# Optimization experiments

Measured on AMD Instinct MI355X. Metric: run time of the kernel, lower is better.

## Reference

```python
import jax, jax.numpy as jnp
import numpy as np

# Predictive-coding graph message passing (PCGraphConv core compute).
# Single-graph edge list (edge_src -> edge_dst) with one scalar weight per edge,
# tiled over the batch (weights.repeat(1, batchsize) in the original).
# PredictionMessagePassing: mu_i = sum_{e: dst(e)=i} w_e * f(x_{src(e)})
# ValueMessagePassing:      dx_j = -eps_j + f'(x_j) * sum_{e: src(e)=j} w_e * eps_{dst(e)}
# with eps = x - mu and f = tanh.

N_PER_GRAPH = 4096
E_PER_GRAPH = 524288
BATCH = 32


def setup_inputs() -> dict:
    key = jax.random.key(0)
    k1, k2, k3, k4 = jax.random.split(key, 4)
    x = jax.random.normal(k1, (BATCH * N_PER_GRAPH,), dtype=jnp.float32)
    weights = jax.random.normal(k2, (E_PER_GRAPH,), dtype=jnp.float32) * (1.0 / np.sqrt(N_PER_GRAPH))
    edge_src = jax.random.randint(k3, (E_PER_GRAPH,), 0, N_PER_GRAPH, dtype=jnp.int32)
    edge_dst = jax.random.randint(k4, (E_PER_GRAPH,), 0, N_PER_GRAPH, dtype=jnp.int32)
    return {"x": x, "weights": weights, "edge_src": edge_src, "edge_dst": edge_dst,
            "batch_size": BATCH, "num_vertices": N_PER_GRAPH}


def reference(x, weights, edge_src, edge_dst, batch_size, num_vertices):
    B, N = batch_size, num_vertices
    BN = B * N
    # Tile single-graph edges across the batch with per-graph node offsets.
    offs = (jnp.arange(B, dtype=edge_src.dtype) * N)[:, None]        # [B,1]
    src = (edge_src[None, :] + offs).reshape(-1)                     # [B*E]
    dst = (edge_dst[None, :] + offs).reshape(-1)                     # [B*E]
    w = jnp.tile(weights, B)                                         # [B*E]

    fx = jnp.tanh(x)                                                 # f(x)
    # Predictions: gather f(x) at src, weight per edge, scatter-add at dst.
    mu = jax.ops.segment_sum(w * fx[src], dst, num_segments=BN)      # [B*N]
    eps = x - mu                                                     # errors
    fprime = 1.0 - fx * fx                                           # f'(x)
    # Value update: backward flow of errors along edges.
    dx = -eps + fprime * jax.ops.segment_sum(w * eps[dst], src, num_segments=BN)
    return jnp.stack([mu, dx])                                       # [2, B*N]
```

## Files before the change

### kernel.cpp

```cpp
#include <hip/hip_runtime.h>


static constexpr int kB = 32, kLogB = 5;
static constexpr int kBkt = 256;
static constexpr int kNPB = 16;
static constexpr int kChunk = 2048;
static constexpr int kTile = 2560;

__global__ void __launch_bounds__(1024) k_hist(
    const int* __restrict__ esrc, const int* __restrict__ edst,
    const float* __restrict__ x, float* __restrict__ x_t,
    float* __restrict__ fx_t, unsigned* __restrict__ cntA,
    unsigned* __restrict__ cntB, int N, int E, int nBB) {
  __shared__ unsigned hA[kBkt], hB[kBkt];
  __shared__ float tile[32][65];
  int tid = threadIdx.x, blk = blockIdx.x;
  if (blk < nBB) {
    if (tid < kBkt) { hA[tid] = 0u; hB[tid] = 0u; }
    __syncthreads();
    int e0 = blk * kChunk, len = min(kChunk, E - e0);
    for (int i = tid; i < len; i += 1024) {
      atomicAdd(&hA[((unsigned)edst[e0 + i]) >> 4], 1u);
      atomicAdd(&hB[((unsigned)esrc[e0 + i]) >> 4], 1u);
    }
    __syncthreads();
    if (tid < kBkt) {
      cntA[(size_t)blk * kBkt + tid] = hA[tid];
      cntB[(size_t)blk * kBkt + tid] = hB[tid];
    }
  } else if (blk - nBB < (N >> 6)) {
    int n0 = (blk - nBB) * 64;
    for (int k = tid; k < 32 * 64; k += 1024) {
      int b = k >> 6, n = k & 63;
      tile[b][n] = x[b * N + n0 + n];
    }
    __syncthreads();
    for (int k = tid; k < 64 * 32; k += 1024) {
      int n = k >> 5, b = k & 31;
      float xv = tile[b][n];
      int j = (n0 + n) * kB + b;
      x_t[j] = xv;
      fx_t[j] = tanhf(xv);
    }
  }
}

__global__ void __launch_bounds__(1024) k_scan(
    const unsigned* __restrict__ cntA, const unsigned* __restrict__ cntB,
    unsigned* __restrict__ baseA, unsigned* __restrict__ baseB,
    unsigned* __restrict__ segA, unsigned* __restrict__ segB, int nBB) {
  __shared__ unsigned qoff[4][kBkt];
  __shared__ unsigned tot[kBkt];
  __shared__ unsigned bb[kBkt];
  const unsigned* cnt = blockIdx.x ? cntB : cntA;
  unsigned* base = blockIdx.x ? baseB : baseA;
  unsigned* seg  = blockIdx.x ? segB  : segA;
  int tid = threadIdx.x;
  int t = tid & (kBkt - 1), q = tid >> 8;
  int qlen = (nBB + 3) >> 2;
  int b0 = q * qlen;
  unsigned run = 0;
  for (int j = 0; j < qlen; j += 8) {
    unsigned c[8];
#pragma unroll
    for (int u = 0; u < 8; ++u) {
      int bi = b0 + j + u;
      c[u] = (bi < nBB) ? cnt[(size_t)bi * kBkt + t] : 0u;
    }
#pragma unroll
    for (int u = 0; u < 8; ++u) run += c[u];
  }
  qoff[q][t] = run;
  __syncthreads();
  unsigned myTot = 0;
  if (tid < kBkt) {
    unsigned p0 = qoff[0][tid], p1 = qoff[1][tid];
    unsigned p2 = qoff[2][tid], p3 = qoff[3][tid];
    qoff[0][tid] = 0u; qoff[1][tid] = p0;
    qoff[2][tid] = p0 + p1; qoff[3][tid] = p0 + p1 + p2;
    myTot = p0 + p1 + p2 + p3;
    tot[tid] = myTot;
  }
  __syncthreads();
  for (int o = 1; o < kBkt; o <<= 1) {
    unsigned v = 0;
    if (tid < kBkt && tid >= o) v = tot[tid - o];
    __syncthreads();
    if (tid < kBkt && tid >= o) tot[tid] += v;
    __syncthreads();
  }
  if (tid < kBkt) {
    unsigned excl = tot[tid] - myTot;
    bb[tid] = excl;
    seg[tid] = excl;
    if (tid == kBkt - 1) seg[kBkt] = excl + myTot;
  }
  __syncthreads();
  run = bb[t] + qoff[q][t];
  for (int j = 0; j < qlen; j += 8) {
    unsigned c[8];
#pragma unroll
    for (int u = 0; u < 8; ++u) {
      int bi = b0 + j + u;
      c[u] = (bi < nBB) ? cnt[(size_t)bi * kBkt + t] : 0u;
    }
#pragma unroll
    for (int u = 0; u < 8; ++u) {
      int bi = b0 + j + u;
      if (bi < nBB) base[(size_t)bi * kBkt + t] = run;
      run += c[u];
    }
  }
}

__global__ void __launch_bounds__(1024) k_scatter(
    const int* __restrict__ esrc, const int* __restrict__ edst,
    const float* __restrict__ wgt,
    const unsigned* __restrict__ cntA, const unsigned* __restrict__ cntB,
    const unsigned* __restrict__ baseA, const unsigned* __restrict__ baseB,
    uint2* __restrict__ recA, uint2* __restrict__ recB, int E, int nBB) {
  __shared__ unsigned myBase[kBkt], cntL[kBkt], baseL[kBkt], cnt2[kBkt];
  __shared__ uint2 cmp[kChunk];
  __shared__ unsigned char bktid[kChunk];
  int tid = threadIdx.x, blk = blockIdx.x;
  int e0 = blk * kChunk, len = min(kChunk, E - e0);
  for (int dir = 0; dir < 2; ++dir) {
    const int* key = dir ? esrc : edst;
    const int* oth = dir ? edst : esrc;
    const unsigned* cnt = dir ? cntB : cntA;
    const unsigned* base = dir ? baseB : baseA;
    uint2* out = dir ? recB : recA;
    if (tid < kBkt) {
      myBase[tid] = base[(size_t)blk * kBkt + tid];
      cntL[tid] = cnt[(size_t)blk * kBkt + tid];
      cnt2[tid] = 0u;
    }
    __syncthreads();
    if (tid < 64) {
      int qq = tid << 2;
      unsigned c0 = cntL[qq], c1 = cntL[qq + 1];
      unsigned c2 = cntL[qq + 2], c3 = cntL[qq + 3];
      unsigned s = c0 + c1 + c2 + c3, run = s;
#pragma unroll
      for (int o = 1; o < 64; o <<= 1) {
        unsigned v = __shfl_up(run, o, 64);
        if (tid >= o) run += v;
      }
      unsigned bse = run - s;
      baseL[qq] = bse; baseL[qq + 1] = bse + c0;
      baseL[qq + 2] = bse + c0 + c1; baseL[qq + 3] = bse + c0 + c1 + c2;
    }
    __syncthreads();
    for (int i = tid; i < len; i += 1024) {
      unsigned ky = (unsigned)key[e0 + i], ot = (unsigned)oth[e0 + i];
      unsigned bbk = ky >> 4;
      unsigned slot = baseL[bbk] + atomicAdd(&cnt2[bbk], 1u);
      cmp[slot] = make_uint2((ot << 4) | (ky & 15u), __float_as_uint(wgt[e0 + i]));
      bktid[slot] = (unsigned char)bbk;
    }
    __syncthreads();
    for (int s = tid; s < len; s += 1024) {
      unsigned bbk = bktid[s];
      out[myBase[bbk] + ((unsigned)s - baseL[bbk])] = cmp[s];
    }
    __syncthreads();
  }
}

__global__ void __launch_bounds__(1024) k_pass(
    const uint2* __restrict__ rec, const unsigned* __restrict__ seg,
    const float* __restrict__ vals, const float* __restrict__ x_t,
    const float* __restrict__ fx_t, float* __restrict__ eps_t,
    float* __restrict__ out, int N, int mode) {
  __shared__ uint2 srt[kTile];
  __shared__ unsigned hW[16 * kNPB];
  __shared__ unsigned wbase[16 * kNPB];
  __shared__ unsigned wcur[16 * kNPB];
  __shared__ unsigned h[kNPB], hb[kNPB];
  __shared__ float red[1024];
  int tid = threadIdx.x, t = blockIdx.x;
  int segb = (int)seg[t], sege = (int)seg[t + 1];
  int wv = tid >> 6;
  int b = tid & 31, hw = tid >> 5, l = hw >> 1, part = hw & 1;
  float acc = 0.0f;

  for (int t0 = segb; t0 < sege; t0 += kTile) {
    int len = min(kTile, sege - t0);
    if (tid < 16 * kNPB) { hW[tid] = 0u; wcur[tid] = 0u; }
    __syncthreads();
    for (int i = tid; i < len; i += 1024)
      atomicAdd(&hW[wv * kNPB + (rec[t0 + i].x & 15u)], 1u);
    __syncthreads();
    if (tid < kNPB) {
      unsigned run = 0;
#pragma unroll
      for (int w2 = 0; w2 < 16; ++w2) {
        unsigned c = hW[w2 * kNPB + tid];
        wbase[w2 * kNPB + tid] = run;
        run += c;
      }
      h[tid] = run;
    }
    __syncthreads();
    if (tid == 0) {
      unsigned run = 0;
#pragma unroll
      for (int l2 = 0; l2 < kNPB; ++l2) { hb[l2] = run; run += h[l2]; }
    }
    __syncthreads();
    if (tid < 16 * kNPB) wbase[tid] += hb[tid & (kNPB - 1)];
    __syncthreads();
    for (int i = tid; i < len; i += 1024) {
      uint2 r = rec[t0 + i];
      unsigned lx = r.x & 15u;
      srt[wbase[wv * kNPB + lx] + atomicAdd(&wcur[wv * kNPB + lx], 1u)] = r;
    }
    __syncthreads();

    int beg = (int)hb[l] + part, end = (int)hb[l] + (int)h[l];
    int last = end - 1; if (last < 0) last = 0;
    uint2 r0, r1, r2, r3, r4, r5, r6, r7;
    float v0, v1, v2, v3, v4, v5, v6, v7;
#define PC_LOAD(d)                                                   \
    { int p = beg + 2 * (d); uint2 rr = srt[min(p, last)];           \
      r##d = rr; v##d = vals[(((rr.x >> 4) & 4095u) << kLogB) + b]; }
    PC_LOAD(0) PC_LOAD(1) PC_LOAD(2) PC_LOAD(3)
    PC_LOAD(4) PC_LOAD(5) PC_LOAD(6) PC_LOAD(7)
#undef PC_LOAD
    int i = beg;
    while (i < end) {
#define PC_STEP(d)                                                   \
      { float wt = (i + 2 * (d) < end) ? __uint_as_float(r##d.y) : 0.0f; \
        acc = fmaf(wt, v##d, acc);                                   \
        int p = i + 16 + 2 * (d); uint2 rr = srt[min(p, last)];      \
        r##d = rr; v##d = vals[(((rr.x >> 4) & 4095u) << kLogB) + b]; }
      PC_STEP(0) PC_STEP(1) PC_STEP(2) PC_STEP(3)
      PC_STEP(4) PC_STEP(5) PC_STEP(6) PC_STEP(7)
#undef PC_STEP
      i += 16;
    }
    __syncthreads();
  }

  red[tid] = acc;
  __syncthreads();
  if (part == 0) {
    float s = red[tid] + red[tid + 32];
    int n = t * kNPB + l;
    int j = (n << kLogB) + b;
    if (mode == 0) {
      out[b * N + n] = s;
      eps_t[j] = x_t[j] - s;
    } else {
      float fx = fx_t[j];
      out[b * N + n] = fmaf(1.0f - fx * fx, s, -eps_t[j]);
    }
  }
}

extern "C" void kernel_launch(void* const* d_in, const int* in_sizes, int n_in,
                              void* d_out, int out_size, void* d_ws, size_t ws_size,
                              hipStream_t stream) {
  const float* x    = (const float*)d_in[0];
  const float* w    = (const float*)d_in[1];
  const int*   esrc = (const int*)d_in[2];
  const int*   edst = (const int*)d_in[3];

  int BN = in_sizes[0];
  int E  = in_sizes[1];
  int N  = BN / kB;
  int nBB = (E + kChunk - 1) / kChunk;

  float* ws    = (float*)d_ws;
  float* x_t   = ws;
  float* fx_t  = ws + (size_t)BN;
  float* eps_t = ws + 2 * (size_t)BN;
  unsigned* cntA = (unsigned*)(ws + 3 * (size_t)BN);
  unsigned* cntB = cntA + (size_t)nBB * kBkt;
  unsigned* baseA = cntB + (size_t)nBB * kBkt;
  unsigned* baseB = baseA + (size_t)nBB * kBkt;
  unsigned* segA = baseB + (size_t)nBB * kBkt;
  unsigned* segB = segA + 512;
  uint2* recA = (uint2*)(segB + 512);
  uint2* recB = recA + (size_t)E;

  float* out_mu = (float*)d_out;
  float* out_dx = (float*)d_out + BN;

  k_hist<<<nBB + (N >> 6), 1024, 0, stream>>>(esrc, edst, x, x_t, fx_t,
                                              cntA, cntB, N, E, nBB);
  k_scan<<<2, 1024, 0, stream>>>(cntA, cntB, baseA, baseB, segA, segB, nBB);
  k_scatter<<<nBB, 1024, 0, stream>>>(esrc, edst, w, cntA, cntB, baseA, baseB,
                                      recA, recB, E, nBB);
  k_pass<<<kBkt, 1024, 0, stream>>>(recA, segA, fx_t, x_t, fx_t,
                                    eps_t, out_mu, N, 0);
  k_pass<<<kBkt, 1024, 0, stream>>>(recB, segB, eps_t, x_t, fx_t,
                                    eps_t, out_dx, N, 1);
}
```

Before: 107.5 us.

## Fuse all five launches into one cooperative persistent kernel with grid syncs

Replaces the histogram, scan, scatter and two pass kernels with a single cooperative kernel of 256 blocks, separated by grid.sync barriers. The edge chunk (src, dst, weight) is staged in shared memory during the histogram phase and reused in the scatter phase, so edges are not reloaded from global memory. The local block histogram is also reused instead of reloading counts. The intent is to remove launch gaps between stages. In exchange, the combined shared-memory footprint is large, which limits residency, and the transpose work is squeezed onto fewer blocks.

Measured after the change: 239.2 us. 123% more time.

```diff
diff --git a/kernel.cpp b/kernel.cpp
--- a/kernel.cpp
+++ b/kernel.cpp
@@ -1,4 +1,7 @@
 #include <hip/hip_runtime.h>
+#include <hip/hip_cooperative_groups.h>
+
+namespace cg = cooperative_groups;
 
 
 static constexpr int kB = 32, kLogB = 5;
@@ -6,179 +9,15 @@
 static constexpr int kNPB = 16;
 static constexpr int kChunk = 2048;
 static constexpr int kTile = 2560;
-
-__global__ void __launch_bounds__(1024) k_hist(
-    const int* __restrict__ esrc, const int* __restrict__ edst,
-    const float* __restrict__ x, float* __restrict__ x_t,
-    float* __restrict__ fx_t, unsigned* __restrict__ cntA,
-    unsigned* __restrict__ cntB, int N, int E, int nBB) {
-  __shared__ unsigned hA[kBkt], hB[kBkt];
-  __shared__ float tile[32][65];
-  int tid = threadIdx.x, blk = blockIdx.x;
-  if (blk < nBB) {
-    if (tid < kBkt) { hA[tid] = 0u; hB[tid] = 0u; }
-    __syncthreads();
-    int e0 = blk * kChunk, len = min(kChunk, E - e0);
-    for (int i = tid; i < len; i += 1024) {
-      atomicAdd(&hA[((unsigned)edst[e0 + i]) >> 4], 1u);
-      atomicAdd(&hB[((unsigned)esrc[e0 + i]) >> 4], 1u);
-    }
-    __syncthreads();
-    if (tid < kBkt) {
-      cntA[(size_t)blk * kBkt + tid] = hA[tid];
-      cntB[(size_t)blk * kBkt + tid] = hB[tid];
-    }
-  } else if (blk - nBB < (N >> 6)) {
-    int n0 = (blk - nBB) * 64;
-    for (int k = tid; k < 32 * 64; k += 1024) {
-      int b = k >> 6, n = k & 63;
-      tile[b][n] = x[b * N + n0 + n];
-    }
-    __syncthreads();
-    for (int k = tid; k < 64 * 32; k += 1024) {
-      int n = k >> 5, b = k & 31;
-      float xv = tile[b][n];
-      int j = (n0 + n) * kB + b;
-      x_t[j] = xv;
-      fx_t[j] = tanhf(xv);
-    }
-  }
-}
-
-__global__ void __launch_bounds__(1024) k_scan(
-    const unsigned* __restrict__ cntA, const unsigned* __restrict__ cntB,
-    unsigned* __restrict__ baseA, unsigned* __restrict__ baseB,
-    unsigned* __restrict__ segA, unsigned* __restrict__ segB, int nBB) {
-  __shared__ unsigned qoff[4][kBkt];
-  __shared__ unsigned tot[kBkt];
-  __shared__ unsigned bb[kBkt];
-  const unsigned* cnt = blockIdx.x ? cntB : cntA;
-  unsigned* base = blockIdx.x ? baseB : baseA;
-  unsigned* seg  = blockIdx.x ? segB  : segA;
-  int tid = threadIdx.x;
-  int t = tid & (kBkt - 1), q = tid >> 8;
-  int qlen = (nBB + 3) >> 2;
-  int b0 = q * qlen;
-  unsigned run = 0;
-  for (int j = 0; j < qlen; j += 8) {
-    unsigned c[8];
-#pragma unroll
-    for (int u = 0; u < 8; ++u) {
-      int bi = b0 + j + u;
-      c[u] = (bi < nBB) ? cnt[(size_t)bi * kBkt + t] : 0u;
-    }
-#pragma unroll
-    for (int u = 0; u < 8; ++u) run += c[u];
-  }
-  qoff[q][t] = run;
-  __syncthreads();
-  unsigned myTot = 0;
-  if (tid < kBkt) {
-    unsigned p0 = qoff[0][tid], p1 = qoff[1][tid];
-    unsigned p2 = qoff[2][tid], p3 = qoff[3][tid];
-    qoff[0][tid] = 0u; qoff[1][tid] = p0;
-    qoff[2][tid] = p0 + p1; qoff[3][tid] = p0 + p1 + p2;
-    myTot = p0 + p1 + p2 + p3;
-    tot[tid] = myTot;
-  }
-  __syncthreads();
-  for (int o = 1; o < kBkt; o <<= 1) {
-    unsigned v = 0;
-    if (tid < kBkt && tid >= o) v = tot[tid - o];
-    __syncthreads();
-    if (tid < kBkt && tid >= o) tot[tid] += v;
-    __syncthreads();
-  }
-  if (tid < kBkt) {
-    unsigned excl = tot[tid] - myTot;
-    bb[tid] = excl;
-    seg[tid] = excl;
-    if (tid == kBkt - 1) seg[kBkt] = excl + myTot;
-  }
-  __syncthreads();
-  run = bb[t] + qoff[q][t];
-  for (int j = 0; j < qlen; j += 8) {
-    unsigned c[8];
-#pragma unroll
-    for (int u = 0; u < 8; ++u) {
-      int bi = b0 + j + u;
-      c[u] = (bi < nBB) ? cnt[(size_t)bi * kBkt + t] : 0u;
-    }
-#pragma unroll
-    for (int u = 0; u < 8; ++u) {
-      int bi = b0 + j + u;
-      if (bi < nBB) base[(size_t)bi * kBkt + t] = run;
-      run += c[u];
-    }
-  }
-}
-
-__global__ void __launch_bounds__(1024) k_scatter(
-    const int* __restrict__ esrc, const int* __restrict__ edst,
-    const float* __restrict__ wgt,
-    const unsigned* __restrict__ cntA, const unsigned* __restrict__ cntB,
-    const unsigned* __restrict__ baseA, const unsigned* __restrict__ baseB,
-    uint2* __restrict__ recA, uint2* __restrict__ recB, int E, int nBB) {
-  __shared__ unsigned myBase[kBkt], cntL[kBkt], baseL[kBkt], cnt2[kBkt];
-  __shared__ uint2 cmp[kChunk];
-  __shared__ unsigned char bktid[kChunk];
-  int tid = threadIdx.x, blk = blockIdx.x;
-  int e0 = blk * kChunk, len = min(kChunk, E - e0);
-  for (int dir = 0; dir < 2; ++dir) {
-    const int* key = dir ? esrc : edst;
-    const int* oth = dir ? edst : esrc;
-    const unsigned* cnt = dir ? cntB : cntA;
-    const unsigned* base = dir ? baseB : baseA;
-    uint2* out = dir ? recB : recA;
-    if (tid < kBkt) {
-      myBase[tid] = base[(size_t)blk * kBkt + tid];
-      cntL[tid] = cnt[(size_t)blk * kBkt + tid];
-      cnt2[tid] = 0u;
-    }
-    __syncthreads();
-    if (tid < 64) {
-      int qq = tid << 2;
-      unsigned c0 = cntL[qq], c1 = cntL[qq + 1];
-      unsigned c2 = cntL[qq + 2], c3 = cntL[qq + 3];
-      unsigned s = c0 + c1 + c2 + c3, run = s;
-#pragma unroll
-      for (int o = 1; o < 64; o <<= 1) {
-        unsigned v = __shfl_up(run, o, 64);
-        if (tid >= o) run += v;
-      }
-      unsigned bse = run - s;
-      baseL[qq] = bse; baseL[qq + 1] = bse + c0;
-      baseL[qq + 2] = bse + c0 + c1; baseL[qq + 3] = bse + c0 + c1 + c2;
-    }
-    __syncthreads();
-    for (int i = tid; i < len; i += 1024) {
-      unsigned ky = (unsigned)key[e0 + i], ot = (unsigned)oth[e0 + i];
-      unsigned bbk = ky >> 4;
-      unsigned slot = baseL[bbk] + atomicAdd(&cnt2[bbk], 1u);
-      cmp[slot] = make_uint2((ot << 4) | (ky & 15u), __float_as_uint(wgt[e0 + i]));
-      bktid[slot] = (unsigned char)bbk;
-    }
-    __syncthreads();
-    for (int s = tid; s < len; s += 1024) {
-      unsigned bbk = bktid[s];
-      out[myBase[bbk] + ((unsigned)s - baseL[bbk])] = cmp[s];
-    }
-    __syncthreads();
-  }
-}
-
-__global__ void __launch_bounds__(1024) k_pass(
+static constexpr int kGrid = 256;
+
+__device__ __forceinline__ void pass_phase(
     const uint2* __restrict__ rec, const unsigned* __restrict__ seg,
     const float* __restrict__ vals, const float* __restrict__ x_t,
     const float* __restrict__ fx_t, float* __restrict__ eps_t,
-    float* __restrict__ out, int N, int mode) {
-  __shared__ uint2 srt[kTile];
-  __shared__ unsigned hW[16 * kNPB];
-  __shared__ unsigned wbase[16 * kNPB];
-  __shared__ unsigned wcur[16 * kNPB];
-  __shared__ unsigned h[kNPB], hb[kNPB];
-  __shared__ float red[1024];
-  int tid = threadIdx.x, t = blockIdx.x;
+    float* __restrict__ out, int N, int mode, int t, int tid,
+    uint2* srt, unsigned* hW, unsigned* wbase, unsigned* wcur,
+    unsigned* h, unsigned* hb, float* red) {
   int segb = (int)seg[t], sege = (int)seg[t + 1];
   int wv = tid >> 6;
   int b = tid & 31, hw = tid >> 5, l = hw >> 1, part = hw & 1;
@@ -256,6 +95,182 @@
       out[b * N + n] = fmaf(1.0f - fx * fx, s, -eps_t[j]);
     }
   }
+  __syncthreads();
+}
+
+__global__ void __launch_bounds__(1024) k_fused(
+    const float* __restrict__ x, const float* __restrict__ w,
+    const int* __restrict__ esrc, const int* __restrict__ edst,
+    float* __restrict__ x_t, float* __restrict__ fx_t,
+    float* __restrict__ eps_t,
+    unsigned* __restrict__ cntA, unsigned* __restrict__ cntB,
+    unsigned* __restrict__ baseA, unsigned* __restrict__ baseB,
+    unsigned* __restrict__ segA, unsigned* __restrict__ segB,
+    uint2* __restrict__ recA, uint2* __restrict__ recB,
+    float* __restrict__ out_mu, float* __restrict__ out_dx,
+    int N, int E, int nBB) {
+  cg::grid_group grid = cg::this_grid();
+
+  __shared__ int sS[kChunk], sD[kChunk];
+  __shared__ float sW[kChunk];
+  __shared__ unsigned hA[kBkt], hB[kBkt];
+  __shared__ unsigned qoff[4][kBkt], tot[kBkt], bbx[kBkt];
+  __shared__ float tile[32][65];
+  __shared__ unsigned myBase[kBkt], baseL[kBkt], cnt2[kBkt];
+  __shared__ uint2 cmp[kChunk];
+  __shared__ unsigned char bktid[kChunk];
+  __shared__ uint2 srt[kTile];
+  __shared__ unsigned hW[16 * kNPB], wbase[16 * kNPB], wcur[16 * kNPB];
+  __shared__ unsigned h[kNPB], hb[kNPB];
+  __shared__ float red[1024];
+
+  int tid = threadIdx.x, blk = blockIdx.x;
+
+  if (blk < nBB) {
+    if (tid < kBkt) { hA[tid] = 0u; hB[tid] = 0u; }
+    __syncthreads();
+    int e0 = blk * kChunk, len = min(kChunk, E - e0);
+    for (int i = tid; i < len; i += 1024) {
+      int s = esrc[e0 + i], d = edst[e0 + i];
+      sS[i] = s; sD[i] = d; sW[i] = w[e0 + i];
+      atomicAdd(&hA[((unsigned)d) >> 4], 1u);
+      atomicAdd(&hB[((unsigned)s) >> 4], 1u);
+    }
+    __syncthreads();
+    if (tid < kBkt) {
+      cntA[(size_t)blk * kBkt + tid] = hA[tid];
+      cntB[(size_t)blk * kBkt + tid] = hB[tid];
+    }
+  }
+  grid.sync();
+
+  if (blk < 2) {
+    const unsigned* cnt = blk ? cntB : cntA;
+    unsigned* base = blk ? baseB : baseA;
+    unsigned* seg  = blk ? segB  : segA;
+    int t = tid & (kBkt - 1), q = tid >> 8;
+    int qlen = (nBB + 3) >> 2;
+    int b0 = q * qlen;
+    unsigned run = 0;
+    for (int j = 0; j < qlen; j += 8) {
+      unsigned c[8];
+#pragma unroll
+      for (int u = 0; u < 8; ++u) {
+        int bi = b0 + j + u;
+        c[u] = (bi < nBB) ? cnt[(size_t)bi * kBkt + t] : 0u;
+      }
+#pragma unroll
+      for (int u = 0; u < 8; ++u) run += c[u];
+    }
+    qoff[q][t] = run;
+    __syncthreads();
+    unsigned myTot = 0;
+    if (tid < kBkt) {
+      unsigned p0 = qoff[0][tid], p1 = qoff[1][tid];
+      unsigned p2 = qoff[2][tid], p3 = qoff[3][tid];
+      qoff[0][tid] = 0u; qoff[1][tid] = p0;
+      qoff[2][tid] = p0 + p1; qoff[3][tid] = p0 + p1 + p2;
+      myTot = p0 + p1 + p2 + p3;
+      tot[tid] = myTot;
+    }
+    __syncthreads();
+    for (int o = 1; o < kBkt; o <<= 1) {
+      unsigned v = 0;
+      if (tid < kBkt && tid >= o) v = tot[tid - o];
+      __syncthreads();
+      if (tid < kBkt && tid >= o) tot[tid] += v;
+      __syncthreads();
+    }
+    if (tid < kBkt) {
+      unsigned excl = tot[tid] - myTot;
+      bbx[tid] = excl;
+      seg[tid] = excl;
+      if (tid == kBkt - 1) seg[kBkt] = excl + myTot;
+    }
+    __syncthreads();
+    run = bbx[t] + qoff[q][t];
+    for (int j = 0; j < qlen; j += 8) {
+      unsigned c[8];
+#pragma unroll
+      for (int u = 0; u < 8; ++u) {
+        int bi = b0 + j + u;
+        c[u] = (bi < nBB) ? cnt[(size_t)bi * kBkt + t] : 0u;
+      }
+#pragma unroll
+      for (int u = 0; u < 8; ++u) {
+        int bi = b0 + j + u;
+        if (bi < nBB) base[(size_t)bi * kBkt + t] = run;
+        run += c[u];
+      }
+    }
+  } else if (blk - 2 < (N >> 6)) {
+    int n0 = (blk - 2) * 64;
+    for (int k = tid; k < 32 * 64; k += 1024) {
+      int b = k >> 6, n = k & 63;
+      tile[b][n] = x[b * N + n0 + n];
+    }
+    __syncthreads();
+    for (int k = tid; k < 64 * 32; k += 1024) {
+      int n = k >> 5, b = k & 31;
+      float xv = tile[b][n];
+      int j = (n0 + n) * kB + b;
+      x_t[j] = xv;
+      fx_t[j] = tanhf(xv);
+    }
+  }
+  grid.sync();
+
+  if (blk < nBB) {
+    int e0 = blk * kChunk, len = min(kChunk, E - e0);
+    for (int dir = 0; dir < 2; ++dir) {
+      const int* key = dir ? sS : sD;
+      const int* oth = dir ? sD : sS;
+      const unsigned* hst = dir ? hB : hA;
+      const unsigned* base = dir ? baseB : baseA;
+      uint2* out = dir ? recB : recA;
+      if (tid < kBkt) {
+        myBase[tid] = base[(size_t)blk * kBkt + tid];
+        cnt2[tid] = 0u;
+      }
+      __syncthreads();
+      if (tid < 64) {
+        int qq = tid << 2;
+        unsigned c0 = hst[qq], c1 = hst[qq + 1];
+        unsigned c2 = hst[qq + 2], c3 = hst[qq + 3];
+        unsigned s = c0 + c1 + c2 + c3, run = s;
+#pragma unroll
+        for (int o = 1; o < 64; o <<= 1) {
+          unsigned v = __shfl_up(run, o, 64);
+          if (tid >= o) run += v;
+        }
+        unsigned bse = run - s;
+        baseL[qq] = bse; baseL[qq + 1] = bse + c0;
+        baseL[qq + 2] = bse + c0 + c1; baseL[qq + 3] = bse + c0 + c1 + c2;
+      }
+      __syncthreads();
+      for (int i = tid; i < len; i += 1024) {
+        unsigned ky = (unsigned)key[i], ot = (unsigned)oth[i];
+        unsigned bbk = ky >> 4;
+        unsigned slot = baseL[bbk] + atomicAdd(&cnt2[bbk], 1u);
+        cmp[slot] = make_uint2((ot << 4) | (ky & 15u), __float_as_uint(sW[i]));
+        bktid[slot] = (unsigned char)bbk;
+      }
+      __syncthreads();
+      for (int s2 = tid; s2 < len; s2 += 1024) {
+        unsigned bbk = bktid[s2];
+        out[myBase[bbk] + ((unsigned)s2 - baseL[bbk])] = cmp[s2];
+      }
+      __syncthreads();
+    }
+  }
+  grid.sync();
+
+  pass_phase(recA, segA, fx_t, x_t, fx_t, eps_t, out_mu, N, 0, blk, tid,
+             srt, hW, wbase, wcur, h, hb, red);
+  grid.sync();
+
+  pass_phase(recB, segB, eps_t, x_t, fx_t, eps_t, out_dx, N, 1, blk, tid,
+             srt, hW, wbase, wcur, h, hb, red);
 }
 
 extern "C" void kernel_launch(void* const* d_in, const int* in_sizes, int n_in,
@@ -287,13 +302,12 @@
   float* out_mu = (float*)d_out;
   float* out_dx = (float*)d_out + BN;
 
-  k_hist<<<nBB + (N >> 6), 1024, 0, stream>>>(esrc, edst, x, x_t, fx_t,
-                                              cntA, cntB, N, E, nBB);
-  k_scan<<<2, 1024, 0, stream>>>(cntA, cntB, baseA, baseB, segA, segB, nBB);
-  k_scatter<<<nBB, 1024, 0, stream>>>(esrc, edst, w, cntA, cntB, baseA, baseB,
-                                      recA, recB, E, nBB);
-  k_pass<<<kBkt, 1024, 0, stream>>>(recA, segA, fx_t, x_t, fx_t,
-                                    eps_t, out_mu, N, 0);
-  k_pass<<<kBkt, 1024, 0, stream>>>(recB, segB, eps_t, x_t, fx_t,
-                                    eps_t, out_dx, N, 1);
+  void* args[] = {
+      (void*)&x, (void*)&w, (void*)&esrc, (void*)&edst,
+      (void*)&x_t, (void*)&fx_t, (void*)&eps_t,
+      (void*)&cntA, (void*)&cntB, (void*)&baseA, (void*)&baseB,
+      (void*)&segA, (void*)&segB, (void*)&recA, (void*)&recB,
+      (void*)&out_mu, (void*)&out_dx, (void*)&N, (void*)&E, (void*)&nBB};
+  hipLaunchCooperativeKernel((void*)k_fused, dim3(kGrid), dim3(1024),
+                             args, 0, stream);
 }
```

## Fuse scan into histogram kernel via last-block atomic counter; stage records in LDS

Applied to the files above, without the earlier changes.

Removes the separate scan kernel launch: each block of the histogram kernel increments a global counter after finishing, and the last two blocks to finish perform the prefix scans for the two edge directions. The counter is cleared with a memset before launch. The pass kernel also stages tile records in shared memory so the global record array is read once instead of twice. The trade-offs are an extra memset, added threadfence and atomic work per block, a scan that now runs in only two blocks at the tail of the kernel, and more LDS per block in the pass kernel.

After: 120.6 us. 1.12x slower.

```diff
diff --git a/kernel.cpp b/kernel.cpp
--- a/kernel.cpp
+++ b/kernel.cpp
@@ -11,10 +11,16 @@
     const int* __restrict__ esrc, const int* __restrict__ edst,
     const float* __restrict__ x, float* __restrict__ x_t,
     float* __restrict__ fx_t, unsigned* __restrict__ cntA,
-    unsigned* __restrict__ cntB, int N, int E, int nBB) {
+    unsigned* __restrict__ cntB,
+    unsigned* __restrict__ baseA, unsigned* __restrict__ baseB,
+    unsigned* __restrict__ segA, unsigned* __restrict__ segB,
+    unsigned* __restrict__ ctr, int N, int E, int nBB, int nTotal) {
   __shared__ unsigned hA[kBkt], hB[kBkt];
   __shared__ float tile[32][65];
+  __shared__ unsigned qoff[4][kBkt], tot[kBkt], bbx[kBkt];
+  __shared__ unsigned rank;
   int tid = threadIdx.x, blk = blockIdx.x;
+
   if (blk < nBB) {
     if (tid < kBkt) { hA[tid] = 0u; hB[tid] = 0u; }
     __syncthreads();
@@ -28,7 +34,7 @@
       cntA[(size_t)blk * kBkt + tid] = hA[tid];
       cntB[(size_t)blk * kBkt + tid] = hB[tid];
     }
-  } else if (blk - nBB < (N >> 6)) {
+  } else {
     int n0 = (blk - nBB) * 64;
     for (int k = tid; k < 32 * 64; k += 1024) {
       int b = k >> 6, n = k & 63;
@@ -43,19 +49,23 @@
       fx_t[j] = tanhf(xv);
     }
   }
-}
-
-__global__ void __launch_bounds__(1024) k_scan(
-    const unsigned* __restrict__ cntA, const unsigned* __restrict__ cntB,
-    unsigned* __restrict__ baseA, unsigned* __restrict__ baseB,
-    unsigned* __restrict__ segA, unsigned* __restrict__ segB, int nBB) {
-  __shared__ unsigned qoff[4][kBkt];
-  __shared__ unsigned tot[kBkt];
-  __shared__ unsigned bb[kBkt];
-  const unsigned* cnt = blockIdx.x ? cntB : cntA;
-  unsigned* base = blockIdx.x ? baseB : baseA;
-  unsigned* seg  = blockIdx.x ? segB  : segA;
-  int tid = threadIdx.x;
+
+  __syncthreads();
+  if (tid == 0) {
+    __threadfence();
+    rank = atomicAdd(ctr, 1u);
+  }
+  __syncthreads();
+  int myRank = (int)rank;
+  int dir = -1;
+  if (myRank == nTotal - 2) dir = 0;
+  if (myRank == nTotal - 1) dir = 1;
+  if (dir < 0) return;
+  __threadfence();
+
+  const unsigned* cnt = dir ? cntB : cntA;
+  unsigned* base = dir ? baseB : baseA;
+  unsigned* seg  = dir ? segB  : segA;
   int t = tid & (kBkt - 1), q = tid >> 8;
   int qlen = (nBB + 3) >> 2;
   int b0 = q * qlen;
@@ -91,12 +101,12 @@
   }
   if (tid < kBkt) {
     unsigned excl = tot[tid] - myTot;
-    bb[tid] = excl;
+    bbx[tid] = excl;
     seg[tid] = excl;
     if (tid == kBkt - 1) seg[kBkt] = excl + myTot;
   }
   __syncthreads();
-  run = bb[t] + qoff[q][t];
+  run = bbx[t] + qoff[q][t];
   for (int j = 0; j < qlen; j += 8) {
     unsigned c[8];
 #pragma unroll
@@ -172,6 +182,7 @@
     const float* __restrict__ vals, const float* __restrict__ x_t,
     const float* __restrict__ fx_t, float* __restrict__ eps_t,
     float* __restrict__ out, int N, int mode) {
+  __shared__ uint2 stg[kTile];
   __shared__ uint2 srt[kTile];
   __shared__ unsigned hW[16 * kNPB];
   __shared__ unsigned wbase[16 * kNPB];
@@ -188,8 +199,11 @@
     int len = min(kTile, sege - t0);
     if (tid < 16 * kNPB) { hW[tid] = 0u; wcur[tid] = 0u; }
     __syncthreads();
-    for (int i = tid; i < len; i += 1024)
-      atomicAdd(&hW[wv * kNPB + (rec[t0 + i].x & 15u)], 1u);
+    for (int i = tid; i < len; i += 1024) {
+      uint2 r = rec[t0 + i];
+      stg[i] = r;
+      atomicAdd(&hW[wv * kNPB + (r.x & 15u)], 1u);
+    }
     __syncthreads();
     if (tid < kNPB) {
       unsigned run = 0;
@@ -211,7 +225,7 @@
     if (tid < 16 * kNPB) wbase[tid] += hb[tid & (kNPB - 1)];
     __syncthreads();
     for (int i = tid; i < len; i += 1024) {
-      uint2 r = rec[t0 + i];
+      uint2 r = stg[i];
       unsigned lx = r.x & 15u;
       srt[wbase[wv * kNPB + lx] + atomicAdd(&wcur[wv * kNPB + lx], 1u)] = r;
     }
@@ -270,6 +284,7 @@
   int E  = in_sizes[1];
   int N  = BN / kB;
   int nBB = (E + kChunk - 1) / kChunk;
+  int nTotal = nBB + (N >> 6);
 
   float* ws    = (float*)d_ws;
   float* x_t   = ws;
@@ -281,15 +296,18 @@
   unsigned* baseB = baseA + (size_t)nBB * kBkt;
   unsigned* segA = baseB + (size_t)nBB * kBkt;
   unsigned* segB = segA + 512;
-  uint2* recA = (uint2*)(segB + 512);
+  unsigned* ctr  = segB + 512;
+  uint2* recA = (uint2*)(ctr + 512);
   uint2* recB = recA + (size_t)E;
 
   float* out_mu = (float*)d_out;
   float* out_dx = (float*)d_out + BN;
 
-  k_hist<<<nBB + (N >> 6), 1024, 0, stream>>>(esrc, edst, x, x_t, fx_t,
-                                              cntA, cntB, N, E, nBB);
-  k_scan<<<2, 1024, 0, stream>>>(cntA, cntB, baseA, baseB, segA, segB, nBB);
+  hipMemsetAsync(ctr, 0, sizeof(unsigned), stream);
+
+  k_hist<<<nTotal, 1024, 0, stream>>>(esrc, edst, x, x_t, fx_t,
+                                      cntA, cntB, baseA, baseB, segA, segB,
+                                      ctr, N, E, nBB, nTotal);
   k_scatter<<<nBB, 1024, 0, stream>>>(esrc, edst, w, cntA, cntB, baseA, baseB,
                                       recA, recB, E, nBB);
   k_pass<<<kBkt, 1024, 0, stream>>>(recA, segA, fx_t, x_t, fx_t,
```

## Split scatter directions and pass buckets across twice as many blocks

Applied to the files above, without the earlier changes.

k_scatter now launches one block per chunk per direction instead of looping over both directions inside a block, doubling the grid. k_pass is split so each 16-node bucket is handled by two 512-thread blocks, each owning 8 nodes. With only 256 buckets the old grid underfilled the 256-CU MI355X, so this aims to raise occupancy and parallelism. The cost is that each k_pass half-block reads the full bucket segment and discards the half it does not own, doubling record reads from global memory.

After: 110.4 us. 1.03x slower.

```diff
diff --git a/kernel.cpp b/kernel.cpp
--- a/kernel.cpp
+++ b/kernel.cpp
@@ -123,81 +123,85 @@
   __shared__ uint2 cmp[kChunk];
   __shared__ unsigned char bktid[kChunk];
   int tid = threadIdx.x, blk = blockIdx.x;
-  int e0 = blk * kChunk, len = min(kChunk, E - e0);
-  for (int dir = 0; dir < 2; ++dir) {
-    const int* key = dir ? esrc : edst;
-    const int* oth = dir ? edst : esrc;
-    const unsigned* cnt = dir ? cntB : cntA;
-    const unsigned* base = dir ? baseB : baseA;
-    uint2* out = dir ? recB : recA;
-    if (tid < kBkt) {
-      myBase[tid] = base[(size_t)blk * kBkt + tid];
-      cntL[tid] = cnt[(size_t)blk * kBkt + tid];
-      cnt2[tid] = 0u;
-    }
-    __syncthreads();
-    if (tid < 64) {
-      int qq = tid << 2;
-      unsigned c0 = cntL[qq], c1 = cntL[qq + 1];
-      unsigned c2 = cntL[qq + 2], c3 = cntL[qq + 3];
-      unsigned s = c0 + c1 + c2 + c3, run = s;
-#pragma unroll
-      for (int o = 1; o < 64; o <<= 1) {
-        unsigned v = __shfl_up(run, o, 64);
-        if (tid >= o) run += v;
-      }
-      unsigned bse = run - s;
-      baseL[qq] = bse; baseL[qq + 1] = bse + c0;
-      baseL[qq + 2] = bse + c0 + c1; baseL[qq + 3] = bse + c0 + c1 + c2;
-    }
-    __syncthreads();
-    for (int i = tid; i < len; i += 1024) {
-      unsigned ky = (unsigned)key[e0 + i], ot = (unsigned)oth[e0 + i];
-      unsigned bbk = ky >> 4;
-      unsigned slot = baseL[bbk] + atomicAdd(&cnt2[bbk], 1u);
-      cmp[slot] = make_uint2((ot << 4) | (ky & 15u), __float_as_uint(wgt[e0 + i]));
-      bktid[slot] = (unsigned char)bbk;
-    }
-    __syncthreads();
-    for (int s = tid; s < len; s += 1024) {
-      unsigned bbk = bktid[s];
-      out[myBase[bbk] + ((unsigned)s - baseL[bbk])] = cmp[s];
-    }
-    __syncthreads();
-  }
-}
-
-__global__ void __launch_bounds__(1024) k_pass(
+  int dir = (blk >= nBB);
+  int c = blk - (dir ? nBB : 0);
+  int e0 = c * kChunk, len = min(kChunk, E - e0);
+  const int* key = dir ? esrc : edst;
+  const int* oth = dir ? edst : esrc;
+  const unsigned* cnt = dir ? cntB : cntA;
+  const unsigned* base = dir ? baseB : baseA;
+  uint2* out = dir ? recB : recA;
+  if (tid < kBkt) {
+    myBase[tid] = base[(size_t)c * kBkt + tid];
+    cntL[tid] = cnt[(size_t)c * kBkt + tid];
+    cnt2[tid] = 0u;
+  }
+  __syncthreads();
+  if (tid < 64) {
+    int qq = tid << 2;
+    unsigned c0 = cntL[qq], c1 = cntL[qq + 1];
+    unsigned c2 = cntL[qq + 2], c3 = cntL[qq + 3];
+    unsigned s = c0 + c1 + c2 + c3, run = s;
+#pragma unroll
+    for (int o = 1; o < 64; o <<= 1) {
+      unsigned v = __shfl_up(run, o, 64);
+      if (tid >= o) run += v;
+    }
+    unsigned bse = run - s;
+    baseL[qq] = bse; baseL[qq + 1] = bse + c0;
+    baseL[qq + 2] = bse + c0 + c1; baseL[qq + 3] = bse + c0 + c1 + c2;
+  }
+  __syncthreads();
+  for (int i = tid; i < len; i += 1024) {
+    unsigned ky = (unsigned)key[e0 + i], ot = (unsigned)oth[e0 + i];
+    unsigned bbk = ky >> 4;
+    unsigned slot = baseL[bbk] + atomicAdd(&cnt2[bbk], 1u);
+    cmp[slot] = make_uint2((ot << 4) | (ky & 15u), __float_as_uint(wgt[e0 + i]));
+    bktid[slot] = (unsigned char)bbk;
+  }
+  __syncthreads();
+  for (int s = tid; s < len; s += 1024) {
+    unsigned bbk = bktid[s];
+    out[myBase[bbk] + ((unsigned)s - baseL[bbk])] = cmp[s];
+  }
+}
+
+__global__ void __launch_bounds__(512) k_pass(
     const uint2* __restrict__ rec, const unsigned* __restrict__ seg,
     const float* __restrict__ vals, const float* __restrict__ x_t,
     const float* __restrict__ fx_t, float* __restrict__ eps_t,
     float* __restrict__ out, int N, int mode) {
   __shared__ uint2 srt[kTile];
-  __shared__ unsigned hW[16 * kNPB];
-  __shared__ unsigned wbase[16 * kNPB];
-  __shared__ unsigned wcur[16 * kNPB];
-  __shared__ unsigned h[kNPB], hb[kNPB];
-  __shared__ float red[1024];
-  int tid = threadIdx.x, t = blockIdx.x;
+  __shared__ unsigned hW[8 * 8];
+  __shared__ unsigned wbase[8 * 8];
+  __shared__ unsigned wcur[8 * 8];
+  __shared__ unsigned h[8], hb[8];
+  __shared__ float red[512];
+  int tid = threadIdx.x;
+  int t = blockIdx.x >> 1, half = blockIdx.x & 1;
   int segb = (int)seg[t], sege = (int)seg[t + 1];
   int wv = tid >> 6;
-  int b = tid & 31, hw = tid >> 5, l = hw >> 1, part = hw & 1;
+  int b = tid & 31, hw = tid >> 5, l3 = hw >> 1, part = hw & 1;
+  unsigned lo8 = (unsigned)half << 3;
   float acc = 0.0f;
 
   for (int t0 = segb; t0 < sege; t0 += kTile) {
     int len = min(kTile, sege - t0);
-    if (tid < 16 * kNPB) { hW[tid] = 0u; wcur[tid] = 0u; }
-    __syncthreads();
-    for (int i = tid; i < len; i += 1024)
-      atomicAdd(&hW[wv * kNPB + (rec[t0 + i].x & 15u)], 1u);
-    __syncthreads();
-    if (tid < kNPB) {
+    if (tid < 64) { hW[tid] = 0u; wcur[tid] = 0u; }
+    __syncthreads();
+    for (int i = tid; i < len; i += 512) {
+      unsigned lx = rec[t0 + i].x & 15u;
+      if ((lx >> 3) == (unsigned)half)
+        atomicAdd(&hW[wv * 8 + (lx & 7u)], 1u);
+    }
+    __syncthreads();
+    if (tid < 8) {
       unsigned run = 0;
 #pragma unroll
-      for (int w2 = 0; w2 < 16; ++w2) {
-        unsigned c = hW[w2 * kNPB + tid];
-        wbase[w2 * kNPB + tid] = run;
-        run += c;
+      for (int w2 = 0; w2 < 8; ++w2) {
+        unsigned cc = hW[w2 * 8 + tid];
+        wbase[w2 * 8 + tid] = run;
+        run += cc;
       }
       h[tid] = run;
     }
@@ -205,19 +209,20 @@
     if (tid == 0) {
       unsigned run = 0;
 #pragma unroll
-      for (int l2 = 0; l2 < kNPB; ++l2) { hb[l2] = run; run += h[l2]; }
-    }
-    __syncthreads();
-    if (tid < 16 * kNPB) wbase[tid] += hb[tid & (kNPB - 1)];
-    __syncthreads();
-    for (int i = tid; i < len; i += 1024) {
+      for (int l2 = 0; l2 < 8; ++l2) { hb[l2] = run; run += h[l2]; }
+    }
+    __syncthreads();
+    if (tid < 64) wbase[tid] += hb[tid & 7];
+    __syncthreads();
+    for (int i = tid; i < len; i += 512) {
       uint2 r = rec[t0 + i];
       unsigned lx = r.x & 15u;
-      srt[wbase[wv * kNPB + lx] + atomicAdd(&wcur[wv * kNPB + lx], 1u)] = r;
-    }
-    __syncthreads();
-
-    int beg = (int)hb[l] + part, end = (int)hb[l] + (int)h[l];
+      if ((lx >> 3) == (unsigned)half)
+        srt[wbase[wv * 8 + (lx & 7u)] + atomicAdd(&wcur[wv * 8 + (lx & 7u)], 1u)] = r;
+    }
+    __syncthreads();
+
+    int beg = (int)hb[l3] + part, end = (int)hb[l3] + (int)h[l3];
     int last = end - 1; if (last < 0) last = 0;
     uint2 r0, r1, r2, r3, r4, r5, r6, r7;
     float v0, v1, v2, v3, v4, v5, v6, v7;
@@ -246,7 +251,7 @@
   __syncthreads();
   if (part == 0) {
     float s = red[tid] + red[tid + 32];
-    int n = t * kNPB + l;
+    int n = t * kNPB + (int)lo8 + l3;
     int j = (n << kLogB) + b;
     if (mode == 0) {
       out[b * N + n] = s;
@@ -290,10 +295,10 @@
   k_hist<<<nBB + (N >> 6), 1024, 0, stream>>>(esrc, edst, x, x_t, fx_t,
                                               cntA, cntB, N, E, nBB);
   k_scan<<<2, 1024, 0, stream>>>(cntA, cntB, baseA, baseB, segA, segB, nBB);
-  k_scatter<<<nBB, 1024, 0, stream>>>(esrc, edst, w, cntA, cntB, baseA, baseB,
-                                      recA, recB, E, nBB);
-  k_pass<<<kBkt, 1024, 0, stream>>>(recA, segA, fx_t, x_t, fx_t,
-                                    eps_t, out_mu, N, 0);
-  k_pass<<<kBkt, 1024, 0, stream>>>(recB, segB, eps_t, x_t, fx_t,
-                                    eps_t, out_dx, N, 1);
-}
+  k_scatter<<<2 * nBB, 1024, 0, stream>>>(esrc, edst, w, cntA, cntB,
+                                          baseA, baseB, recA, recB, E, nBB);
+  k_pass<<<2 * kBkt, 512, 0, stream>>>(recA, segA, fx_t, x_t, fx_t,
+                                       eps_t, out_mu, N, 0);
+  k_pass<<<2 * kBkt, 512, 0, stream>>>(recB, segB, eps_t, x_t, fx_t,
+                                       eps_t, out_dx, N, 1);
+}
```
